# Optimization experiments

Hardware: AMD Instinct MI355X
Metric: run time of the kernel (lower is better)

The kernel has to match this reference:

```python
import jax, jax.numpy as jnp
import numpy as np
import math

B, T, C = 4, 2048, 1024
N_HEAD = 16
HEAD = C // N_HEAD  # 64
ROPE_BASE = 10000.0


def rotate_half(x):
    x1, x2 = x[..., : x.shape[-1] // 2], x[..., x.shape[-1] // 2:]
    return jnp.concatenate((-x2, x1), axis=-1)


def rope_cos_sin(seq_len, dim, dtype=jnp.float32):
    inv_freq = 1.0 / (ROPE_BASE ** (jnp.arange(0, dim, 2, dtype=jnp.float32) / dim))
    t = jnp.arange(seq_len, dtype=jnp.float32)
    freqs = jnp.einsum('i,j->ij', t, inv_freq)          # [T, dim/2]
    emb = jnp.concatenate((freqs, freqs), axis=-1)       # [T, dim]
    return jnp.cos(emb).astype(dtype), jnp.sin(emb).astype(dtype)


def setup_inputs() -> dict:
    key = jax.random.key(0)
    ks = jax.random.split(key, 5)
    s_in = 1.0 / math.sqrt(C)
    return {
        'x': jax.random.normal(ks[0], (B, T, C), dtype=jnp.float32),
        'W_qkv': jax.random.normal(ks[1], (C, 3 * C), dtype=jnp.float32) * s_in,
        'b_qkv': jnp.zeros((3 * C,), dtype=jnp.float32),
        'W_proj': jax.random.normal(ks[2], (C, C), dtype=jnp.float32) * s_in,
        'b_proj': jnp.zeros((C,), dtype=jnp.float32),
    }


def reference(x, W_qkv, b_qkv, W_proj, b_proj):
    b, t, c = x.shape
    qkv = x @ W_qkv + b_qkv                               # [B,T,3C]
    q, k, v = jnp.split(qkv, 3, axis=-1)
    # [B,T,C] -> [B,H,T,hd]
    def to_heads(u):
        return u.reshape(b, t, N_HEAD, HEAD).transpose(0, 2, 1, 3)
    q, k, v = to_heads(q), to_heads(k), to_heads(v)
    # RoPE
    cos, sin = rope_cos_sin(t, HEAD, x.dtype)             # [T,hd]
    cos = cos[None, None]; sin = sin[None, None]
    q = q * cos + rotate_half(q) * sin
    k = k * cos + rotate_half(k) * sin
    # naive causal attention (materializes [B,H,T,T] like the original)
    att = jnp.einsum('bhqd,bhkd->bhqk', q, k) * (1.0 / math.sqrt(HEAD))
    causal = jnp.tril(jnp.ones((t, t), dtype=bool))
    att = jnp.where(causal[None, None], att, -jnp.inf)
    att = jax.nn.softmax(att, axis=-1)
    y = jnp.einsum('bhqk,bhkd->bhqd', att, v)             # [B,H,T,hd]
    y = y.transpose(0, 2, 1, 3).reshape(b, t, c)
    return y @ W_proj + b_proj
```

## Files before the change

### kernel.cpp

```cpp
#include <hip/hip_runtime.h>
#include <stdint.h>

#define B_  4
#define T_  2048
#define C_  1024
#define NH_ 16
#define HD_ 64
#define BH_ (B_*NH_)
#define M_  (B_*T_)

using f32x4  = __attribute__((ext_vector_type(4))) float;
using f32x16 = __attribute__((ext_vector_type(16))) float;
using bf16x8 = __attribute__((ext_vector_type(8))) short;

__device__ __forceinline__ unsigned short f2bf(float x) {
  union { float f; uint32_t u; } v; v.f = x;
  uint32_t u = v.u;
  return (unsigned short)((u + 0x7FFFu + ((u >> 16) & 1u)) >> 16);
}

__device__ __forceinline__ uint32_t cvtpk(float a, float b) {
  uint32_t r;
  asm("v_cvt_pk_bf16_f32 %0, %1, %2" : "=v"(r) : "v"(a), "v"(b));
  return r;
}

__device__ __forceinline__ void gload16(const void* g, void* l) {
  __builtin_amdgcn_global_load_lds(
      (const __attribute__((address_space(1))) void*)g,
      (__attribute__((address_space(3))) void*)l, 16, 0, 0);
}


__global__ void k_cvt_bf16(const float* __restrict__ src,
                           unsigned short* __restrict__ dst, int n) {
  int i = (blockIdx.x * 256 + threadIdx.x) * 4;
  if (i + 3 < n) {
    float4 v = *(const float4*)(src + i);
    ushort4 o;
    o.x = f2bf(v.x); o.y = f2bf(v.y); o.z = f2bf(v.z); o.w = f2bf(v.w);
    *(ushort4*)(dst + i) = o;
  }
}

__global__ void k_transpose_w(const float* __restrict__ W,
                              unsigned short* __restrict__ WT, int K, int N) {
  __shared__ float tile[32][33];
  int bx = blockIdx.x, by = blockIdx.y;
  int tx = threadIdx.x, ty = threadIdx.y;
  #pragma unroll
  for (int i = 0; i < 32; i += 8)
    tile[ty + i][tx] = W[(size_t)(by*32 + ty + i) * N + bx*32 + tx];
  __syncthreads();
  #pragma unroll
  for (int i = 0; i < 32; i += 8)
    WT[(size_t)(bx*32 + ty + i) * K + by*32 + tx] = f2bf(tile[tx][ty + i]);
}

__global__ void k_rope_tab(float* __restrict__ cosT, float* __restrict__ sinT) {
  int t = blockIdx.x * 8 + threadIdx.y;
  int i = threadIdx.x;
  float inv = expf(-(float)i * (9.210340371976184f / 32.0f));
  float f = (float)t * inv;
  cosT[t*32 + i] = cosf(f);
  sinT[t*32 + i] = sinf(f);
}

template<int N, int K, int EPI>
__global__ __launch_bounds__(256)
void k_gemm(const unsigned short* __restrict__ A,
            const unsigned short* __restrict__ BT,
            const float* __restrict__ bias,
            const float* __restrict__ cosT,
            const float* __restrict__ sinT,
            unsigned short* __restrict__ Qh,
            unsigned short* __restrict__ Kh,
            unsigned short* __restrict__ VhT,
            float* __restrict__ outF) {
  __shared__ alignas(16) unsigned short As[128*64];
  __shared__ alignas(16) unsigned short Bs[128*64];
  const int tid  = threadIdx.x;
  const int lane = tid & 63;
  const int wv   = tid >> 6;
  const int wm   = wv >> 1, wn = wv & 1;
  const int m0   = blockIdx.y * 128;
  const int n0   = blockIdx.x * 128;
  const int l15  = lane & 15, l4 = lane >> 4;

  f32x4 acc[4][4] = {};

  for (int kt = 0; kt < K/64; ++kt) {
    __syncthreads();
    #pragma unroll
    for (int it = 0; it < 4; ++it) {
      int idx  = it*256 + wv*64 + lane;
      int row  = idx >> 3, slot = idx & 7;
      int g    = slot ^ (row & 7);
      const unsigned short* ga = A  + ((size_t)(m0 + row) * K + kt*64 + g*8);
      const unsigned short* gb = BT + ((size_t)(n0 + row) * K + kt*64 + g*8);
      gload16(ga, (void*)(As + (it*256 + wv*64) * 8));
      gload16(gb, (void*)(Bs + (it*256 + wv*64) * 8));
    }
    __syncthreads();
    #pragma unroll
    for (int ks = 0; ks < 2; ++ks) {
      bf16x8 af[4], bfr[4];
      #pragma unroll
      for (int mi = 0; mi < 4; ++mi) {
        int r = wm*64 + mi*16 + l15;
        int g = (ks*4 + l4) ^ (r & 7);
        af[mi] = *(const bf16x8*)(As + r*64 + g*8);
      }
      #pragma unroll
      for (int ni = 0; ni < 4; ++ni) {
        int r = wn*64 + ni*16 + l15;
        int g = (ks*4 + l4) ^ (r & 7);
        bfr[ni] = *(const bf16x8*)(Bs + r*64 + g*8);
      }
      #pragma unroll
      for (int mi = 0; mi < 4; ++mi)
        #pragma unroll
        for (int ni = 0; ni < 4; ++ni)
          acc[mi][ni] = __builtin_amdgcn_mfma_f32_16x16x32_bf16(
              af[mi], bfr[ni], acc[mi][ni], 0, 0, 0);
    }
  }

  if (EPI == 0) {
    const int ncol = n0 + wn*64;
    const int part = ncol >> 10;
    const int hid  = (ncol & 1023) >> 6;
    unsigned short* dstQK = (part == 0) ? Qh : Kh;
    #pragma unroll
    for (int mi = 0; mi < 4; ++mi) {
      #pragma unroll
      for (int j = 0; j < 4; ++j) {
        int row = m0 + wm*64 + mi*16 + l4*4 + j;
        int bb = row >> 11, tt = row & 2047;
        if (part < 2) {
          size_t base = ((size_t)((bb*NH_ + hid) * T_ + tt)) * HD_;
          #pragma unroll
          for (int ni = 0; ni < 2; ++ni) {
            int d = ni*16 + l15;
            float a1 = acc[mi][ni][j]     + bias[ncol + d];
            float a2 = acc[mi][ni + 2][j] + bias[ncol + d + 32];
            float cv = cosT[tt*32 + d], sv = sinT[tt*32 + d];
            float o1 = a1*cv - a2*sv;
            float o2 = a2*cv + a1*sv;
            if (part == 0) { o1 *= 0.18033688011112042f; o2 *= 0.18033688011112042f; }
            dstQK[base + d]      = f2bf(o1);
            dstQK[base + d + 32] = f2bf(o2);
          }
        } else {
          #pragma unroll
          for (int ni = 0; ni < 4; ++ni) {
            int d = ni*16 + l15;
            float av = acc[mi][ni][j] + bias[ncol + d];
            VhT[((size_t)((bb*NH_ + hid) * HD_ + d)) * T_ + tt] = f2bf(av);
          }
        }
      }
    }
  } else {
    #pragma unroll
    for (int mi = 0; mi < 4; ++mi)
      #pragma unroll
      for (int ni = 0; ni < 4; ++ni)
        #pragma unroll
        for (int j = 0; j < 4; ++j) {
          int row = m0 + wm*64 + mi*16 + l4*4 + j;
          int col = n0 + wn*64 + ni*16 + l15;
          outF[(size_t)row * N + col] = acc[mi][ni][j] + bias[col];
        }
  }
}

__global__ __launch_bounds__(256, 3)
void k_attn(const unsigned short* __restrict__ Qh,
            const unsigned short* __restrict__ Kh,
            const unsigned short* __restrict__ VhT,
            unsigned short* __restrict__ Y) {
  __shared__ alignas(16) unsigned short Ks[2][64*64];
  __shared__ alignas(16) unsigned short Vs[2][64*64];
  const int tid  = threadIdx.x;
  const int lane = tid & 63;
  const int wv   = tid >> 6;
  const int l31  = lane & 31;
  const int h    = lane >> 5;
  const int bh   = blockIdx.x & 63;
  const int qb   = 15 - (blockIdx.x >> 6);
  const int r32  = qb*128 + wv*32;
  const int nt   = 2*qb + 2;
  const int qg   = r32 + l31;

  bf16x8 qf[4];
  #pragma unroll
  for (int i = 0; i < 4; ++i)
    qf[i] = *(const bf16x8*)(Qh + ((size_t)(bh*T_ + qg))*HD_ + i*16 + h*8);

  float m_r = -1e30f, l_r = 0.f;
  f32x16 o[2] = {};

  auto stage = [&](int buf, int jt) {
    #pragma unroll
    for (int it = 0; it < 2; ++it) {
      int idx = it*256 + wv*64 + lane;
      int row = idx >> 3, slot = idx & 7;
      int g   = slot ^ (row & 7);
      gload16(Kh  + ((size_t)(bh*T_ + jt*64 + row))*HD_ + g*8,
              (void*)(Ks[buf] + (it*256 + wv*64)*8));
      gload16(VhT + ((size_t)(bh*HD_ + row))*T_ + jt*64 + g*8,
              (void*)(Vs[buf] + (it*256 + wv*64)*8));
    }
  };

  stage(0, 0);
  int cur = 0;

  for (int jt = 0; jt < nt; ++jt) {
    if (jt + 1 < nt) {
      stage(cur ^ 1, jt + 1);
      asm volatile("s_waitcnt vmcnt(4)" ::: "memory");
    } else {
      asm volatile("s_waitcnt vmcnt(0)" ::: "memory");
    }
    __builtin_amdgcn_s_barrier();
    asm volatile("" ::: "memory");

    if (jt*64 <= r32 + 31) {
      f32x16 s[2] = {f32x16{0}, f32x16{0}};
      __builtin_amdgcn_s_setprio(1);
      #pragma unroll
      for (int kb = 0; kb < 2; ++kb)
        #pragma unroll
        for (int i = 0; i < 4; ++i) {
          int r = kb*32 + l31;
          int g = (2*i + h) ^ (r & 7);
          bf16x8 kf = *(const bf16x8*)(Ks[cur] + r*64 + g*8);
          s[kb] = __builtin_amdgcn_mfma_f32_32x32x16_bf16(kf, qf[i], s[kb], 0, 0, 0);
        }
      __builtin_amdgcn_s_setprio(0);

      float p[2][16];
      const bool diag = (jt + 1)*64 > r32;
      #pragma unroll
      for (int kb = 0; kb < 2; ++kb)
        #pragma unroll
        for (int r = 0; r < 16; ++r) {
          float v = s[kb][r];
          if (diag) {
            int key = jt*64 + kb*32 + (r & 3) + 8*(r >> 2) + 4*h;
            v = (key > qg) ? -1e30f : v;
          }
          p[kb][r] = v;
        }

      float mx[16];
      #pragma unroll
      for (int r = 0; r < 16; ++r) mx[r] = fmaxf(p[0][r], p[1][r]);
      #pragma unroll
      for (int st = 8; st > 0; st >>= 1)
        #pragma unroll
        for (int r = 0; r < 8; ++r)
          if (r < st) mx[r] = fmaxf(mx[r], mx[r + st]);
      float tm = fmaxf(mx[0], __shfl_xor(mx[0], 32));

      if (!__all(tm <= m_r + 8.0f)) {
        float mn = fmaxf(m_r, tm);
        float scale = exp2f(m_r - mn);
        m_r = mn;
        l_r *= scale;
        #pragma unroll
        for (int dblk = 0; dblk < 2; ++dblk)
          #pragma unroll
          for (int r = 0; r < 16; ++r)
            o[dblk][r] *= scale;
      }

      #pragma unroll
      for (int kb = 0; kb < 2; ++kb)
        #pragma unroll
        for (int r = 0; r < 16; ++r)
          p[kb][r] = exp2f(p[kb][r] - m_r);

      float sm[16];
      #pragma unroll
      for (int r = 0; r < 16; ++r) sm[r] = p[0][r] + p[1][r];
      #pragma unroll
      for (int st = 8; st > 0; st >>= 1)
        #pragma unroll
        for (int r = 0; r < 8; ++r)
          if (r < st) sm[r] += sm[r + st];
      l_r += sm[0] + __shfl_xor(sm[0], 32);

      #pragma unroll
      for (int kb = 0; kb < 2; ++kb) {
        uint32_t a01 = cvtpk(p[kb][0],  p[kb][1]);
        uint32_t a23 = cvtpk(p[kb][2],  p[kb][3]);
        uint32_t a45 = cvtpk(p[kb][4],  p[kb][5]);
        uint32_t a67 = cvtpk(p[kb][6],  p[kb][7]);
        uint32_t b01 = cvtpk(p[kb][8],  p[kb][9]);
        uint32_t b23 = cvtpk(p[kb][10], p[kb][11]);
        uint32_t b45 = cvtpk(p[kb][12], p[kb][13]);
        uint32_t b67 = cvtpk(p[kb][14], p[kb][15]);
        uint32_t s1 = h ? a01 : a45, s2 = h ? a23 : a67;
        uint32_t s3 = h ? b01 : b45, s4 = h ? b23 : b67;
        uint32_t x1 = __shfl_xor(s1, 32), x2 = __shfl_xor(s2, 32);
        uint32_t x3 = __shfl_xor(s3, 32), x4 = __shfl_xor(s4, 32);
        union { bf16x8 v; uint32_t d[4]; } f0, f1;
        f0.d[0] = h ? x1 : a01;  f0.d[1] = h ? x2 : a23;
        f0.d[2] = h ? a45 : x1;  f0.d[3] = h ? a67 : x2;
        f1.d[0] = h ? x3 : b01;  f1.d[1] = h ? x4 : b23;
        f1.d[2] = h ? b45 : x3;  f1.d[3] = h ? b67 : x4;

        __builtin_amdgcn_s_setprio(1);
        #pragma unroll
        for (int koff = 0; koff < 2; ++koff) {
          bf16x8 pf = koff ? f1.v : f0.v;
          #pragma unroll
          for (int dblk = 0; dblk < 2; ++dblk) {
            int rv = dblk*32 + l31;
            int gv = (kb*4 + koff*2 + h) ^ (rv & 7);
            bf16x8 vf = *(const bf16x8*)(Vs[cur] + rv*64 + gv*8);
            o[dblk] = __builtin_amdgcn_mfma_f32_32x32x16_bf16(vf, pf, o[dblk], 0, 0, 0);
          }
        }
        __builtin_amdgcn_s_setprio(0);
      }
    }

    __syncthreads();
    cur ^= 1;
  }

  int b = bh >> 4, hd = bh & 15;
  float rinv = 1.0f / l_r;
  unsigned short* yrow = Y + ((size_t)(b*T_ + r32 + l31))*C_ + hd*64;
  #pragma unroll
  for (int dblk = 0; dblk < 2; ++dblk)
    #pragma unroll
    for (int g2 = 0; g2 < 4; ++g2) {
      ushort4 o4;
      o4.x = f2bf(o[dblk][g2*4 + 0] * rinv);
      o4.y = f2bf(o[dblk][g2*4 + 1] * rinv);
      o4.z = f2bf(o[dblk][g2*4 + 2] * rinv);
      o4.w = f2bf(o[dblk][g2*4 + 3] * rinv);
      *(ushort4*)(yrow + dblk*32 + g2*8 + 4*h) = o4;
    }
}


extern "C" void kernel_launch(void* const* d_in, const int* in_sizes, int n_in,
                              void* d_out, int out_size, void* d_ws, size_t ws_size,
                              hipStream_t stream) {
  const float* x      = (const float*)d_in[0];
  const float* W_qkv  = (const float*)d_in[1];
  const float* b_qkv  = (const float*)d_in[2];
  const float* W_proj = (const float*)d_in[3];
  const float* b_proj = (const float*)d_in[4];
  float* out = (float*)d_out;

  char* ws = (char*)d_ws;
  size_t off = 0;
  auto alloc = [&](size_t bytes) {
    void* p = ws + off; off += (bytes + 255) & ~(size_t)255; return p;
  };
  unsigned short* xb     = (unsigned short*)alloc((size_t)M_ * C_ * 2);
  unsigned short* WqkvT  = (unsigned short*)alloc((size_t)3 * C_ * C_ * 2);
  unsigned short* WprojT = (unsigned short*)alloc((size_t)C_ * C_ * 2);
  unsigned short* Qh     = (unsigned short*)alloc((size_t)M_ * C_ * 2);
  unsigned short* Kh     = (unsigned short*)alloc((size_t)M_ * C_ * 2);
  unsigned short* VhT    = (unsigned short*)alloc((size_t)M_ * C_ * 2);
  float* cosT = (float*)alloc((size_t)T_ * 32 * 4);
  float* sinT = (float*)alloc((size_t)T_ * 32 * 4);
  unsigned short* Y = xb;

  k_cvt_bf16<<<(M_*C_/4 + 255)/256, 256, 0, stream>>>(x, xb, M_*C_);
  dim3 tb(32, 8);
  k_transpose_w<<<dim3(3*C_/32, C_/32), tb, 0, stream>>>(W_qkv, WqkvT, C_, 3*C_);
  k_transpose_w<<<dim3(C_/32,   C_/32), tb, 0, stream>>>(W_proj, WprojT, C_, C_);
  k_rope_tab<<<T_/8, tb, 0, stream>>>(cosT, sinT);

  k_gemm<3*C_, C_, 0><<<dim3(3*C_/128, M_/128), 256, 0, stream>>>(
      xb, WqkvT, b_qkv, cosT, sinT, Qh, Kh, VhT, nullptr);

  k_attn<<<dim3(T_/128 * BH_), 256, 0, stream>>>(Qh, Kh, VhT, Y);

  k_gemm<C_, C_, 1><<<dim3(C_/128, M_/128), 256, 0, stream>>>(
      Y, WprojT, b_proj, nullptr, nullptr, nullptr, nullptr, nullptr, out);
}
```

Before: 213.0 us.

## Replace GEMM with 256x256 double-buffered, phase-interleaved MFMA kernel

Replaces the 128x128 single-buffered GEMM with a 512-thread, 256x256-tile kernel. Its two LDS buffers are filled by global_load_lds in quarter-tile stages that are interleaved with MFMA phases under explicit barriers, vmcnt waits and s_setprio. It also remaps block IDs across 8 groups so neighbouring blocks share A/B tiles in cache. The goal is to hide global load latency and raise data reuse per LDS byte. The cost is much larger LDS use (128 KB per block), heavy barrier use, and fewer blocks for the projection GEMM (128), which may underfill the CUs.

Result: slower. 263.8 us (+23.8%).

```diff
diff --git a/kernel.cpp b/kernel.cpp
--- a/kernel.cpp
+++ b/kernel.cpp
@@ -8,6 +8,7 @@
 #define HD_ 64
 #define BH_ (B_*NH_)
 #define M_  (B_*T_)
+#define KT_ 16
 
 using f32x4  = __attribute__((ext_vector_type(4))) float;
 using f32x16 = __attribute__((ext_vector_type(16))) float;
@@ -30,6 +31,10 @@
       (const __attribute__((address_space(1))) void*)g,
       (__attribute__((address_space(3))) void*)l, 16, 0, 0);
 }
+
+#define BAR() do { asm volatile("" ::: "memory"); __builtin_amdgcn_s_barrier(); \
+                   asm volatile("" ::: "memory"); } while (0)
+#define VMC(N) asm volatile("s_waitcnt vmcnt(" #N ")" ::: "memory")
 
 
 __global__ void k_cvt_bf16(const float* __restrict__ src,
@@ -66,112 +71,184 @@
   sinT[t*32 + i] = sinf(f);
 }
 
-template<int N, int K, int EPI>
-__global__ __launch_bounds__(256)
-void k_gemm(const unsigned short* __restrict__ A,
-            const unsigned short* __restrict__ BT,
-            const float* __restrict__ bias,
-            const float* __restrict__ cosT,
-            const float* __restrict__ sinT,
-            unsigned short* __restrict__ Qh,
-            unsigned short* __restrict__ Kh,
-            unsigned short* __restrict__ VhT,
-            float* __restrict__ outF) {
-  __shared__ alignas(16) unsigned short As[128*64];
-  __shared__ alignas(16) unsigned short Bs[128*64];
+
+#define LDA(BUF, QR) do { \
+  const unsigned short* _b = As[BUF]; \
+  _Pragma("unroll") for (int mi = 0; mi < 4; ++mi) \
+  _Pragma("unroll") for (int ks = 0; ks < 2; ++ks) { \
+    int r = wr*128 + (QR)*64 + mi*16 + l15; \
+    af[mi][ks] = *(const bf16x8*)(_b + r*64 + (((ks*4 + l4) ^ (r & 7))*8)); } \
+} while (0)
+
+#define LDB(BUF, QC, BQ) do { \
+  const unsigned short* _b = Bs[BUF]; \
+  _Pragma("unroll") for (int ni = 0; ni < 2; ++ni) \
+  _Pragma("unroll") for (int ks = 0; ks < 2; ++ks) { \
+    int n = wc*64 + (QC)*32 + ni*16 + l15; \
+    BQ[ni][ks] = *(const bf16x8*)(_b + n*64 + (((ks*4 + l4) ^ (n & 7))*8)); } \
+} while (0)
+
+#define MM(QR, QC, BQ) do { \
+  __builtin_amdgcn_s_setprio(1); \
+  _Pragma("unroll") for (int ks = 0; ks < 2; ++ks) \
+  _Pragma("unroll") for (int mi = 0; mi < 4; ++mi) \
+  _Pragma("unroll") for (int ni = 0; ni < 2; ++ni) \
+    acc[QR][QC][mi][ni] = __builtin_amdgcn_mfma_f32_16x16x32_bf16( \
+        af[mi][ks], BQ[ni][ks], acc[QR][QC][mi][ni], 0, 0, 0); \
+  __builtin_amdgcn_s_setprio(0); \
+} while (0)
+
+#define STAGE_A(BUF, T, U) do { \
+  int _t = (T) < KT_ ? (T) : KT_-1; \
+  _Pragma("unroll") for (int rI = 0; rI < 2; ++rI) { \
+    int rowb = rI*128 + (U)*64 + wv*8; \
+    int row  = rowb + (lane >> 3); \
+    int g    = (lane & 7) ^ (row & 7); \
+    gload16(Ag + (size_t)(m0 + row)*1024 + _t*64 + g*8, \
+            (void*)(As[BUF] + rowb*64)); } \
+} while (0)
+
+#define STAGE_B(BUF, T, U) do { \
+  int _t = (T) < KT_ ? (T) : KT_-1; \
+  _Pragma("unroll") for (int rI = 0; rI < 2; ++rI) { \
+    int nb = rI*128 + (U)*32 + wv*8 + (wv & 4)*8; \
+    int n  = nb + (lane >> 3); \
+    int g  = (lane & 7) ^ (n & 7); \
+    gload16(Bg + (size_t)(n0 + n)*1024 + _t*64 + g*8, \
+            (void*)(Bs[BUF] + nb*64)); } \
+} while (0)
+
+template<int N, int EPI>
+__global__ __launch_bounds__(512, 2)
+void k_gemm256(const unsigned short* __restrict__ Ag,
+               const unsigned short* __restrict__ Bg,
+               const float* __restrict__ bias,
+               const float* __restrict__ cosT,
+               const float* __restrict__ sinT,
+               unsigned short* __restrict__ Qh,
+               unsigned short* __restrict__ Kh,
+               unsigned short* __restrict__ VhT,
+               float* __restrict__ outF) {
+  __shared__ alignas(16) unsigned short As[2][256*64];
+  __shared__ alignas(16) unsigned short Bs[2][256*64];
   const int tid  = threadIdx.x;
   const int lane = tid & 63;
   const int wv   = tid >> 6;
-  const int wm   = wv >> 1, wn = wv & 1;
-  const int m0   = blockIdx.y * 128;
-  const int n0   = blockIdx.x * 128;
+  const int wr   = wv >> 2, wc = wv & 3;
   const int l15  = lane & 15, l4 = lane >> 4;
-
-  f32x4 acc[4][4] = {};
-
-  for (int kt = 0; kt < K/64; ++kt) {
-    __syncthreads();
-    #pragma unroll
-    for (int it = 0; it < 4; ++it) {
-      int idx  = it*256 + wv*64 + lane;
-      int row  = idx >> 3, slot = idx & 7;
-      int g    = slot ^ (row & 7);
-      const unsigned short* ga = A  + ((size_t)(m0 + row) * K + kt*64 + g*8);
-      const unsigned short* gb = BT + ((size_t)(n0 + row) * K + kt*64 + g*8);
-      gload16(ga, (void*)(As + (it*256 + wv*64) * 8));
-      gload16(gb, (void*)(Bs + (it*256 + wv*64) * 8));
-    }
-    __syncthreads();
-    #pragma unroll
-    for (int ks = 0; ks < 2; ++ks) {
-      bf16x8 af[4], bfr[4];
-      #pragma unroll
-      for (int mi = 0; mi < 4; ++mi) {
-        int r = wm*64 + mi*16 + l15;
-        int g = (ks*4 + l4) ^ (r & 7);
-        af[mi] = *(const bf16x8*)(As + r*64 + g*8);
-      }
-      #pragma unroll
-      for (int ni = 0; ni < 4; ++ni) {
-        int r = wn*64 + ni*16 + l15;
-        int g = (ks*4 + l4) ^ (r & 7);
-        bfr[ni] = *(const bf16x8*)(Bs + r*64 + g*8);
-      }
-      #pragma unroll
-      for (int mi = 0; mi < 4; ++mi)
-        #pragma unroll
-        for (int ni = 0; ni < 4; ++ni)
-          acc[mi][ni] = __builtin_amdgcn_mfma_f32_16x16x32_bf16(
-              af[mi], bfr[ni], acc[mi][ni], 0, 0, 0);
-    }
+  const int nwg = gridDim.x, cpx = nwg >> 3;
+  const int id  = ((int)blockIdx.x & 7) * cpx + ((int)blockIdx.x >> 3);
+  const int m0  = (id & 31) * 256;
+  const int n0  = (id >> 5) * 256;
+
+  f32x4  acc[2][2][4][2] = {};
+  bf16x8 af[4][2], bq0[2][2], bq1[2][2];
+
+  STAGE_A(0, 0, 0); STAGE_B(0, 0, 0); STAGE_B(0, 0, 1); STAGE_A(0, 0, 1);
+  STAGE_B(1, 1, 0); STAGE_B(1, 1, 1); STAGE_A(1, 1, 1);
+  VMC(6);
+  BAR();
+
+  for (int i = 0; i < KT_/2; ++i) {
+    const int t1 = 2*i + 1;
+    const int t2 = 2*i + 2;
+    const int t3 = 2*i + 3;
+    LDA(0, 0); LDB(0, 0, bq0);
+    STAGE_A(1, t1, 0);
+    BAR();
+    MM(0, 0, bq0);
+    BAR();
+    LDB(0, 1, bq1);
+    STAGE_B(0, t2, 0);
+    BAR();
+    MM(0, 1, bq1);
+    BAR();
+    LDA(0, 1);
+    STAGE_B(0, t2, 1);
+    BAR();
+    MM(1, 0, bq0);
+    BAR();
+    STAGE_A(0, t2, 1);
+    BAR();
+    MM(1, 1, bq1);
+    VMC(6);
+    BAR();
+    LDA(1, 0); LDB(1, 0, bq0);
+    STAGE_A(0, t2, 0);
+    BAR();
+    MM(0, 0, bq0);
+    BAR();
+    LDB(1, 1, bq1);
+    STAGE_B(1, t3, 0);
+    BAR();
+    MM(0, 1, bq1);
+    BAR();
+    LDA(1, 1);
+    STAGE_B(1, t3, 1);
+    BAR();
+    MM(1, 0, bq0);
+    BAR();
+    STAGE_A(1, t3, 1);
+    BAR();
+    MM(1, 1, bq1);
+    VMC(6);
+    BAR();
   }
+  VMC(0);
 
   if (EPI == 0) {
-    const int ncol = n0 + wn*64;
-    const int part = ncol >> 10;
-    const int hid  = (ncol & 1023) >> 6;
+    const int nc   = n0 + wc*64;
+    const int part = nc >> 10;
+    const int hid  = (nc & 1023) >> 6;
     unsigned short* dstQK = (part == 0) ? Qh : Kh;
     #pragma unroll
-    for (int mi = 0; mi < 4; ++mi) {
-      #pragma unroll
-      for (int j = 0; j < 4; ++j) {
-        int row = m0 + wm*64 + mi*16 + l4*4 + j;
-        int bb = row >> 11, tt = row & 2047;
-        if (part < 2) {
-          size_t base = ((size_t)((bb*NH_ + hid) * T_ + tt)) * HD_;
-          #pragma unroll
-          for (int ni = 0; ni < 2; ++ni) {
-            int d = ni*16 + l15;
-            float a1 = acc[mi][ni][j]     + bias[ncol + d];
-            float a2 = acc[mi][ni + 2][j] + bias[ncol + d + 32];
-            float cv = cosT[tt*32 + d], sv = sinT[tt*32 + d];
-            float o1 = a1*cv - a2*sv;
-            float o2 = a2*cv + a1*sv;
-            if (part == 0) { o1 *= 0.18033688011112042f; o2 *= 0.18033688011112042f; }
-            dstQK[base + d]      = f2bf(o1);
-            dstQK[base + d + 32] = f2bf(o2);
-          }
-        } else {
-          #pragma unroll
-          for (int ni = 0; ni < 4; ++ni) {
-            int d = ni*16 + l15;
-            float av = acc[mi][ni][j] + bias[ncol + d];
-            VhT[((size_t)((bb*NH_ + hid) * HD_ + d)) * T_ + tt] = f2bf(av);
+    for (int qr = 0; qr < 2; ++qr)
+      #pragma unroll
+      for (int mi = 0; mi < 4; ++mi)
+        #pragma unroll
+        for (int j = 0; j < 4; ++j) {
+          int row = m0 + wr*128 + qr*64 + mi*16 + l4*4 + j;
+          int bb = row >> 11, tt = row & 2047;
+          if (part < 2) {
+            size_t base = ((size_t)((bb*NH_ + hid) * T_ + tt)) * HD_;
+            #pragma unroll
+            for (int ni = 0; ni < 2; ++ni) {
+              int d = ni*16 + l15;
+              float a1 = acc[qr][0][mi][ni][j] + bias[nc + d];
+              float a2 = acc[qr][1][mi][ni][j] + bias[nc + d + 32];
+              float cv = cosT[tt*32 + d], sv = sinT[tt*32 + d];
+              float o1 = a1*cv - a2*sv;
+              float o2 = a2*cv + a1*sv;
+              if (part == 0) { o1 *= 0.18033688011112042f; o2 *= 0.18033688011112042f; }
+              dstQK[base + d]      = f2bf(o1);
+              dstQK[base + d + 32] = f2bf(o2);
+            }
+          } else {
+            #pragma unroll
+            for (int qc = 0; qc < 2; ++qc)
+              #pragma unroll
+              for (int ni = 0; ni < 2; ++ni) {
+                int d = qc*32 + ni*16 + l15;
+                float av = acc[qr][qc][mi][ni][j] + bias[nc + d];
+                VhT[((size_t)((bb*NH_ + hid) * HD_ + d)) * T_ + tt] = f2bf(av);
+              }
           }
         }
-      }
-    }
   } else {
     #pragma unroll
-    for (int mi = 0; mi < 4; ++mi)
-      #pragma unroll
-      for (int ni = 0; ni < 4; ++ni)
-        #pragma unroll
-        for (int j = 0; j < 4; ++j) {
-          int row = m0 + wm*64 + mi*16 + l4*4 + j;
-          int col = n0 + wn*64 + ni*16 + l15;
-          outF[(size_t)row * N + col] = acc[mi][ni][j] + bias[col];
-        }
+    for (int qr = 0; qr < 2; ++qr)
+      #pragma unroll
+      for (int qc = 0; qc < 2; ++qc)
+        #pragma unroll
+        for (int mi = 0; mi < 4; ++mi)
+          #pragma unroll
+          for (int ni = 0; ni < 2; ++ni)
+            #pragma unroll
+            for (int j = 0; j < 4; ++j) {
+              int row = m0 + wr*128 + qr*64 + mi*16 + l4*4 + j;
+              int col = n0 + wc*64 + qc*32 + ni*16 + l15;
+              outF[(size_t)row * N + col] = acc[qr][qc][mi][ni][j] + bias[col];
+            }
   }
 }
 
@@ -381,11 +458,11 @@
   k_transpose_w<<<dim3(C_/32,   C_/32), tb, 0, stream>>>(W_proj, WprojT, C_, C_);
   k_rope_tab<<<T_/8, tb, 0, stream>>>(cosT, sinT);
 
-  k_gemm<3*C_, C_, 0><<<dim3(3*C_/128, M_/128), 256, 0, stream>>>(
+  k_gemm256<3*C_, 0><<<dim3(32*12), 512, 0, stream>>>(
       xb, WqkvT, b_qkv, cosT, sinT, Qh, Kh, VhT, nullptr);
 
   k_attn<<<dim3(T_/128 * BH_), 256, 0, stream>>>(Qh, Kh, VhT, Y);
 
-  k_gemm<C_, C_, 1><<<dim3(C_/128, M_/128), 256, 0, stream>>>(
+  k_gemm256<C_, 1><<<dim3(32*4), 512, 0, stream>>>(
       Y, WprojT, b_proj, nullptr, nullptr, nullptr, nullptr, nullptr, out);
 }
```

## Double-buffer GEMM LDS tiles and remap blocks across XCDs

Applied to the files above, without the earlier changes.

The GEMM kernel now uses double-buffered LDS tiles, so it issues the next K-tile's global-to-LDS loads before computing on the current one and waits with a partial vmcnt. Launches become a 1D grid with a block-id permutation that spreads neighbouring tiles across the 8 XCDs, which may improve L2 locality. MFMA sections get raised wave priority. The goal is to hide global load latency behind matrix math, at the cost of doubling LDS use to 64KB per block, which may lower occupancy.

After: 211.7 us. Within noise of the previous version (-0.6%).

```diff
diff --git a/kernel.cpp b/kernel.cpp
--- a/kernel.cpp
+++ b/kernel.cpp
@@ -30,6 +30,10 @@
       (const __attribute__((address_space(1))) void*)g,
       (__attribute__((address_space(3))) void*)l, 16, 0, 0);
 }
+
+#define BAR() do { asm volatile("" ::: "memory"); __builtin_amdgcn_s_barrier(); \
+                   asm volatile("" ::: "memory"); } while (0)
+#define VMC(N) asm volatile("s_waitcnt vmcnt(" #N ")" ::: "memory")
 
 
 __global__ void k_cvt_bf16(const float* __restrict__ src,
@@ -68,7 +72,7 @@
 
 template<int N, int K, int EPI>
 __global__ __launch_bounds__(256)
-void k_gemm(const unsigned short* __restrict__ A,
+void k_gemm(const unsigned short* __restrict__ Ag,
             const unsigned short* __restrict__ BT,
             const float* __restrict__ bias,
             const float* __restrict__ cosT,
@@ -77,31 +81,44 @@
             unsigned short* __restrict__ Kh,
             unsigned short* __restrict__ VhT,
             float* __restrict__ outF) {
-  __shared__ alignas(16) unsigned short As[128*64];
-  __shared__ alignas(16) unsigned short Bs[128*64];
+  __shared__ alignas(16) unsigned short As[2][128*64];
+  __shared__ alignas(16) unsigned short Bs[2][128*64];
   const int tid  = threadIdx.x;
   const int lane = tid & 63;
   const int wv   = tid >> 6;
   const int wm   = wv >> 1, wn = wv & 1;
-  const int m0   = blockIdx.y * 128;
-  const int n0   = blockIdx.x * 128;
   const int l15  = lane & 15, l4 = lane >> 4;
+  const int NT  = N / 128;
+  const int id  = ((int)blockIdx.x & 7) * ((int)gridDim.x >> 3) + ((int)blockIdx.x >> 3);
+  const int m0  = (id / NT) * 128;
+  const int n0  = (id % NT) * 128;
 
   f32x4 acc[4][4] = {};
 
-  for (int kt = 0; kt < K/64; ++kt) {
-    __syncthreads();
+  auto stage = [&](int buf, int kt) {
     #pragma unroll
     for (int it = 0; it < 4; ++it) {
       int idx  = it*256 + wv*64 + lane;
       int row  = idx >> 3, slot = idx & 7;
       int g    = slot ^ (row & 7);
-      const unsigned short* ga = A  + ((size_t)(m0 + row) * K + kt*64 + g*8);
-      const unsigned short* gb = BT + ((size_t)(n0 + row) * K + kt*64 + g*8);
-      gload16(ga, (void*)(As + (it*256 + wv*64) * 8));
-      gload16(gb, (void*)(Bs + (it*256 + wv*64) * 8));
-    }
-    __syncthreads();
+      gload16(Ag + (size_t)(m0 + row) * K + kt*64 + g*8,
+              (void*)(As[buf] + (it*256 + wv*64) * 8));
+      gload16(BT + (size_t)(n0 + row) * K + kt*64 + g*8,
+              (void*)(Bs[buf] + (it*256 + wv*64) * 8));
+    }
+  };
+
+  stage(0, 0);
+  int cur = 0;
+
+  for (int kt = 0; kt < K/64; ++kt) {
+    if (kt + 1 < K/64) {
+      stage(cur ^ 1, kt + 1);
+      VMC(8);
+    } else {
+      VMC(0);
+    }
+    BAR();
     #pragma unroll
     for (int ks = 0; ks < 2; ++ks) {
       bf16x8 af[4], bfr[4];
@@ -109,21 +126,25 @@
       for (int mi = 0; mi < 4; ++mi) {
         int r = wm*64 + mi*16 + l15;
         int g = (ks*4 + l4) ^ (r & 7);
-        af[mi] = *(const bf16x8*)(As + r*64 + g*8);
+        af[mi] = *(const bf16x8*)(As[cur] + r*64 + g*8);
       }
       #pragma unroll
       for (int ni = 0; ni < 4; ++ni) {
         int r = wn*64 + ni*16 + l15;
         int g = (ks*4 + l4) ^ (r & 7);
-        bfr[ni] = *(const bf16x8*)(Bs + r*64 + g*8);
+        bfr[ni] = *(const bf16x8*)(Bs[cur] + r*64 + g*8);
       }
+      __builtin_amdgcn_s_setprio(1);
       #pragma unroll
       for (int mi = 0; mi < 4; ++mi)
         #pragma unroll
         for (int ni = 0; ni < 4; ++ni)
           acc[mi][ni] = __builtin_amdgcn_mfma_f32_16x16x32_bf16(
               af[mi], bfr[ni], acc[mi][ni], 0, 0, 0);
-    }
+      __builtin_amdgcn_s_setprio(0);
+    }
+    BAR();
+    cur ^= 1;
   }
 
   if (EPI == 0) {
@@ -220,12 +241,11 @@
   for (int jt = 0; jt < nt; ++jt) {
     if (jt + 1 < nt) {
       stage(cur ^ 1, jt + 1);
-      asm volatile("s_waitcnt vmcnt(4)" ::: "memory");
+      VMC(4);
     } else {
-      asm volatile("s_waitcnt vmcnt(0)" ::: "memory");
-    }
-    __builtin_amdgcn_s_barrier();
-    asm volatile("" ::: "memory");
+      VMC(0);
+    }
+    BAR();
 
     if (jt*64 <= r32 + 31) {
       f32x16 s[2] = {f32x16{0}, f32x16{0}};
@@ -329,7 +349,7 @@
       }
     }
 
-    __syncthreads();
+    BAR();
     cur ^= 1;
   }
 
@@ -381,11 +401,11 @@
   k_transpose_w<<<dim3(C_/32,   C_/32), tb, 0, stream>>>(W_proj, WprojT, C_, C_);
   k_rope_tab<<<T_/8, tb, 0, stream>>>(cosT, sinT);
 
-  k_gemm<3*C_, C_, 0><<<dim3(3*C_/128, M_/128), 256, 0, stream>>>(
+  k_gemm<3*C_, C_, 0><<<dim3(1536), 256, 0, stream>>>(
       xb, WqkvT, b_qkv, cosT, sinT, Qh, Kh, VhT, nullptr);
 
   k_attn<<<dim3(T_/128 * BH_), 256, 0, stream>>>(Qh, Kh, VhT, Y);
 
-  k_gemm<C_, C_, 1><<<dim3(C_/128, M_/128), 256, 0, stream>>>(
+  k_gemm<C_, C_, 1><<<dim3(512), 256, 0, stream>>>(
       Y, WprojT, b_proj, nullptr, nullptr, nullptr, nullptr, nullptr, out);
 }
```
